# Kernel optimization log

Hardware: AMD Instinct MI355X
Metric: run time of the kernel (lower is better)

The kernel has to match this reference:

```python
import jax, jax.numpy as jnp
import numpy as np

EMA = 0.99
THRESH = 0.8
EPS = 1e-8


def setup_inputs() -> dict:
    key = jax.random.key(0)
    k1, k2, k3, k4 = jax.random.split(key, 4)
    B, C, M = 8192, 2048, 8192
    return {
        "features": jax.random.normal(k1, (B, C), dtype=jnp.float32),
        "confidence": jax.random.uniform(k2, (B,), dtype=jnp.float32),
        "mem_features": jax.random.normal(k3, (M, C), dtype=jnp.float32),
        "mem_confidences": jax.random.uniform(k4, (M,), dtype=jnp.float32),
        "ptr0": 4096,
        "filled0": 4096,
    }


def _update(mem_feat, mem_conf, ptr0, filled0, features, confidence):
    M = mem_feat.shape[0]

    def step(carry, xs):
        mf, mc, ptr, filled = carry
        feat, conf = xs
        is_high = conf > THRESH
        p = jnp.mod(ptr, M)
        exists = filled > p
        cur_f = mf[p]          # [C]
        cur_c = mc[p]
        upd_f = jnp.where(exists, EMA * cur_f + (1.0 - EMA) * feat, feat)
        upd_c = jnp.where(exists, EMA * cur_c + (1.0 - EMA) * conf, conf)
        new_f = jnp.where(is_high, upd_f, cur_f)
        new_c = jnp.where(is_high, upd_c, cur_c)
        mf = mf.at[p].set(new_f)
        mc = mc.at[p].set(new_c)
        filled = filled + jnp.where(is_high & (~exists), 1, 0).astype(filled.dtype)
        ptr = ptr + jnp.where(is_high, 1, 0).astype(ptr.dtype)
        return (mf, mc, ptr, filled), None

    init = (mem_feat, mem_conf,
            jnp.asarray(ptr0, jnp.int32), jnp.asarray(filled0, jnp.int32))
    (mf, mc, ptr, filled), _ = jax.lax.scan(step, init, (features, confidence))
    return mf, mc, filled


def reference(features, confidence, mem_features, mem_confidences, ptr0, filled0):
    mf, mc, filled = _update(mem_features, mem_confidences, ptr0, filled0,
                             features, confidence)
    M, C = mf.shape
    # confidence-weighted stats over valid slots [:filled] (mask, jit-safe)
    valid = (jnp.arange(M) < filled).astype(mf.dtype)
    w = mc * valid                              # [M]
    total = jnp.sum(w) + EPS
    mean = jnp.einsum("mc,m->c", mf, w) / total  # [C]
    diff = mf - mean[None, :]
    var = jnp.einsum("mc,m->c", diff * diff, w) / total
    std = jnp.sqrt(var + EPS)
    # pack: updated memory bank + weighted mean + weighted std -> [M+2, C]
    return jnp.concatenate([mf, mean[None, :], std[None, :]], axis=0)
```

## Files before the change

kernel.cpp:

```cpp
#include <hip/hip_runtime.h>
#include <math.h>

#define EMA_A 0.99f
#define EMA_B 0.01f
#define THRESH 0.8f
#define EPS_F 1e-8f

#define NBLK2 512
#define RPB   16

typedef float fx4 __attribute__((ext_vector_type(4)));


__global__ __launch_bounds__(1024)
void k_scan(const float* __restrict__ conf,
            const int* __restrict__ ptr0_p,
            const int* __restrict__ filled0_p,
            int* __restrict__ hdr,
            int* __restrict__ slot_info,
            int B, int M)
{
    const int tid  = threadIdx.x;
    const int lane = tid & 63;

    for (int m = tid; m < M; m += 1024) slot_info[m] = -1;

    const int base_i = tid * 8;
    int mask = 0;
    #pragma unroll
    for (int k = 0; k < 8; ++k) {
        int i = base_i + k;
        float c = (i < B) ? conf[i] : 0.0f;
        mask |= (c > THRESH) ? (1 << k) : 0;
    }
    int cnt = __popc(mask);

    __shared__ int s_cnt[1024];
    __shared__ int s_gbase[64];
    s_cnt[tid] = cnt;
    __syncthreads();

    if (tid < 64) {
        int sum16 = 0;
        #pragma unroll
        for (int u = 0; u < 16; ++u) sum16 += s_cnt[tid * 16 + u];
        int v = sum16;
        #pragma unroll
        for (int d = 1; d < 64; d <<= 1) {
            int o = __shfl_up(v, d, 64);
            if (lane >= d) v += o;
        }
        s_gbase[tid] = v - sum16;
        if (tid == 63) hdr[0] = v;
    }
    __syncthreads();
    const int K = hdr[0];

    int j = s_gbase[tid >> 4];
    for (int u = (tid & ~15); u < tid; ++u) j += s_cnt[u];

    int P0 = ((ptr0_p[0] % M) + M) % M;
    int F0 = filled0_p[0];
    if (F0 < 0) F0 = 0;
    if (F0 > M) F0 = M;
    const int L0 = M - P0;
    const int F1 = F0 + (M - (P0 > F0 ? P0 : F0));

    #pragma unroll
    for (int k = 0; k < 8; ++k) {
        if (mask & (1 << k)) {
            int exist;
            if (j < L0)          exist = (P0 + j) < F0 ? 1 : 0;
            else if (j < L0 + M) exist = (j - L0) < F1 ? 1 : 0;
            else                 exist = 1;
            int p = (P0 + j) % M;
            slot_info[p] = ((base_i + k) << 1) | exist;
            ++j;
        }
    }

    if (tid == 0) {
        int n0 = K < L0 ? K : L0;
        int e0 = F0 - P0; if (e0 < 0) e0 = 0; if (e0 > n0) e0 = n0;
        int fresh0 = n0 - e0;
        int n1 = K - L0; if (n1 < 0) n1 = 0; if (n1 > M) n1 = M;
        int fresh1 = n1 - F1; if (fresh1 < 0) fresh1 = 0;
        int filled = F0 + fresh0 + fresh1;
        if (filled > M) filled = M;
        hdr[1] = filled;
    }
}


__global__ __launch_bounds__(512)
void k_update(const float* __restrict__ mem_feat,
              const float* __restrict__ feat,
              const float* __restrict__ conf,
              const float* __restrict__ mem_conf,
              const int* __restrict__ slot_info,
              const int* __restrict__ hdr,
              float* __restrict__ out,
              float* __restrict__ p0,
              float* __restrict__ p1,
              float* __restrict__ p2,
              int C)
{
    const int blk = blockIdx.x, tid = threadIdx.x;
    const int c0 = tid * 4;

    __shared__ int   s_info[RPB];
    __shared__ float s_w[RPB];
    const int row0 = blk * RPB;
    if (tid < RPB) {
        const int m = row0 + tid;
        const int info = slot_info[m];
        const int filled = hdr[1];
        const float mco = mem_conf[m];
        float mcu = mco;
        if (info >= 0) {
            float c = conf[info >> 1];
            mcu = (info & 1) ? (EMA_A * mco + EMA_B * c) : c;
        }
        s_info[tid] = info;
        s_w[tid]    = (m < filled) ? mcu : 0.0f;
    }
    __syncthreads();
    if (tid == 0) {
        float s = 0.0f;
        #pragma unroll
        for (int r = 0; r < RPB; ++r) s += s_w[r];
        p0[blk] = s;
    }

    fx4 s1 = {0.f, 0.f, 0.f, 0.f};
    fx4 s2 = {0.f, 0.f, 0.f, 0.f};

    #pragma unroll 4
    for (int r = 0; r < RPB; ++r) {
        const int m = row0 + r;
        const size_t base = (size_t)m * C;
        const int info = s_info[r];
        fx4 x;
        if (info < 0) {
            x = *(const fx4*)(mem_feat + base + c0);
        } else if (info & 1) {
            fx4 mv = *(const fx4*)(mem_feat + base + c0);
            fx4 fv = *(const fx4*)(feat + (size_t)(info >> 1) * C + c0);
            x = EMA_A * mv + EMA_B * fv;
        } else {
            x = *(const fx4*)(feat + (size_t)(info >> 1) * C + c0);
        }
        const float wv = s_w[r];
        s1 += wv * x;
        s2 += wv * x * x;
        __builtin_nontemporal_store(x, (fx4*)(out + base + c0));
    }
    const size_t pb = (size_t)blk * C;
    *(fx4*)(p1 + pb + c0) = s1;
    *(fx4*)(p2 + pb + c0) = s2;
}


__global__ __launch_bounds__(256)
void k_stats(const float* __restrict__ p0,
             const float* __restrict__ p1,
             const float* __restrict__ p2,
             float* __restrict__ out,
             int M, int C)
{
    const int tid = threadIdx.x;

    __shared__ float s_sw[4];
    float sw = 0.0f;
    for (int i = tid; i < NBLK2; i += 256) sw += p0[i];
    #pragma unroll
    for (int d = 32; d >= 1; d >>= 1) sw += __shfl_down(sw, d, 64);
    if ((tid & 63) == 0) s_sw[tid >> 6] = sw;
    __syncthreads();

    const int cc = tid & 31;
    const int chunk = tid >> 5;
    const int c = blockIdx.x * 32 + cc;
    double s1 = 0.0, s2 = 0.0;
    for (int bb = 0; bb < NBLK2 / 8; ++bb) {
        int b = chunk * (NBLK2 / 8) + bb;
        s1 += (double)p1[(size_t)b * C + c];
        s2 += (double)p2[(size_t)b * C + c];
    }
    __shared__ double l1[256], l2[256];
    l1[tid] = s1;
    l2[tid] = s2;
    __syncthreads();
    if (chunk == 0) {
        for (int q = 1; q < 8; ++q) { s1 += l1[cc + 32 * q]; s2 += l2[cc + 32 * q]; }
        double sumw  = (double)(s_sw[0] + s_sw[1] + s_sw[2] + s_sw[3]);
        double total = sumw + (double)EPS_F;
        double mean  = s1 / total;
        double var   = (s2 - 2.0 * mean * s1 + mean * mean * sumw) / total;
        out[(size_t)M * C + c]       = (float)mean;
        out[(size_t)(M + 1) * C + c] = (float)sqrt(var + (double)EPS_F);
    }
}


extern "C" void kernel_launch(void* const* d_in, const int* in_sizes, int n_in,
                              void* d_out, int out_size, void* d_ws, size_t ws_size,
                              hipStream_t stream)
{
    const float* features     = (const float*)d_in[0];
    const float* confidence   = (const float*)d_in[1];
    const float* mem_features = (const float*)d_in[2];
    const float* mem_conf     = (const float*)d_in[3];
    const int*   ptr0         = (const int*)d_in[4];
    const int*   filled0      = (const int*)d_in[5];

    const int B = in_sizes[1];
    const int M = in_sizes[3];
    const int C = in_sizes[0] / B;

    char* ws = (char*)d_ws;
    int*   hdr       = (int*)ws;
    int*   slot_info = (int*)(ws + 1024);
    float* p0        = (float*)(ws + 1024 + 4 * (size_t)M);
    float* p1        = (float*)(ws + 65536);
    float* p2        = (float*)(ws + 65536 + 4 * (size_t)NBLK2 * C);

    float* out = (float*)d_out;

    k_scan<<<1, 1024, 0, stream>>>(confidence, ptr0, filled0, hdr, slot_info, B, M);
    k_update<<<NBLK2, 512, 0, stream>>>(mem_features, features, confidence, mem_conf,
                                        slot_info, hdr, out, p0, p1, p2, C);
    k_stats<<<C / 32, 256, 0, stream>>>(p0, p1, p2, out, M, C);
}
```

Baseline: 185.6 us.

## Replace per-block partial sums with global float atomics and a light finalize kernel

The update kernel now accumulates weighted sums directly into global arrays with float atomicAdd, instead of writing per-block partials that a separate stats kernel re-reads. Each block doubles its threads, splits the rows between two halves, and combines the halves through shared memory before issuing the atomics. The row source pointer is also precomputed per row so the inner loop has fewer branches. This removes the partial-buffer round trip and the heavier reduction kernel, at the cost of many atomic operations per column, non-deterministic float summation order, and reduced precision compared with the old double-precision reduction. The zeroing of the global accumulators is folded into the scan kernel.

```diff
diff --git a/kernel.cpp b/kernel.cpp
--- a/kernel.cpp
+++ b/kernel.cpp
@@ -18,12 +18,16 @@
             const int* __restrict__ filled0_p,
             int* __restrict__ hdr,
             int* __restrict__ slot_info,
-            int B, int M)
+            float* __restrict__ g_sumw,
+            float* __restrict__ g1,
+            int B, int M, int C)
 {
     const int tid  = threadIdx.x;
     const int lane = tid & 63;
 
     for (int m = tid; m < M; m += 1024) slot_info[m] = -1;
+    for (int i = tid; i < 2 * C; i += 1024) g1[i] = 0.0f;
+    if (tid == 0) *g_sumw = 0.0f;
 
     const int base_i = tid * 8;
     int mask = 0;
@@ -92,7 +96,7 @@
 }
 
 
-__global__ __launch_bounds__(512)
+__global__ __launch_bounds__(1024)
 void k_update(const float* __restrict__ mem_feat,
               const float* __restrict__ feat,
               const float* __restrict__ conf,
@@ -100,103 +104,94 @@
               const int* __restrict__ slot_info,
               const int* __restrict__ hdr,
               float* __restrict__ out,
-              float* __restrict__ p0,
-              float* __restrict__ p1,
-              float* __restrict__ p2,
+              float* __restrict__ g_sumw,
+              float* __restrict__ g1,
+              float* __restrict__ g2,
               int C)
 {
-    const int blk = blockIdx.x, tid = threadIdx.x;
-    const int c0 = tid * 4;
-
-    __shared__ int   s_info[RPB];
+    const int blk  = blockIdx.x, tid = threadIdx.x;
+    const int half = tid >> 9;
+    const int c4   = tid & 511;
+    const int c0   = c4 * 4;
+    const int row0 = blk * RPB;
+
+    __shared__ const float* s_src[RPB];
+    __shared__ int   s_ema[RPB];
     __shared__ float s_w[RPB];
-    const int row0 = blk * RPB;
+
     if (tid < RPB) {
         const int m = row0 + tid;
         const int info = slot_info[m];
         const int filled = hdr[1];
         const float mco = mem_conf[m];
         float mcu = mco;
+        const float* src = mem_feat + (size_t)m * C;
+        int ema = 0;
         if (info >= 0) {
-            float c = conf[info >> 1];
-            mcu = (info & 1) ? (EMA_A * mco + EMA_B * c) : c;
-        }
-        s_info[tid] = info;
-        s_w[tid]    = (m < filled) ? mcu : 0.0f;
+            const float c = conf[info >> 1];
+            src = feat + (size_t)(info >> 1) * C;
+            if (info & 1) { mcu = EMA_A * mco + EMA_B * c; ema = 1; }
+            else          { mcu = c; }
+        }
+        s_src[tid] = src;
+        s_ema[tid] = ema;
+        s_w[tid]   = (m < filled) ? mcu : 0.0f;
     }
     __syncthreads();
     if (tid == 0) {
         float s = 0.0f;
         #pragma unroll
         for (int r = 0; r < RPB; ++r) s += s_w[r];
-        p0[blk] = s;
+        atomicAdd(g_sumw, s);
     }
 
     fx4 s1 = {0.f, 0.f, 0.f, 0.f};
     fx4 s2 = {0.f, 0.f, 0.f, 0.f};
 
-    #pragma unroll 4
-    for (int r = 0; r < RPB; ++r) {
+    #pragma unroll
+    for (int rr = 0; rr < RPB / 2; ++rr) {
+        const int r = rr * 2 + half;
         const int m = row0 + r;
-        const size_t base = (size_t)m * C;
-        const int info = s_info[r];
-        fx4 x;
-        if (info < 0) {
-            x = *(const fx4*)(mem_feat + base + c0);
-        } else if (info & 1) {
-            fx4 mv = *(const fx4*)(mem_feat + base + c0);
-            fx4 fv = *(const fx4*)(feat + (size_t)(info >> 1) * C + c0);
-            x = EMA_A * mv + EMA_B * fv;
-        } else {
-            x = *(const fx4*)(feat + (size_t)(info >> 1) * C + c0);
+        fx4 x = *(const fx4*)(s_src[r] + c0);
+        if (s_ema[r]) {
+            fx4 mv = *(const fx4*)(mem_feat + (size_t)m * C + c0);
+            x = EMA_A * mv + EMA_B * x;
         }
         const float wv = s_w[r];
         s1 += wv * x;
         s2 += wv * x * x;
-        __builtin_nontemporal_store(x, (fx4*)(out + base + c0));
-    }
-    const size_t pb = (size_t)blk * C;
-    *(fx4*)(p1 + pb + c0) = s1;
-    *(fx4*)(p2 + pb + c0) = s2;
+        __builtin_nontemporal_store(x, (fx4*)(out + (size_t)m * C + c0));
+    }
+
+    __shared__ fx4 st1[512], st2[512];
+    if (half == 1) { st1[c4] = s1; st2[c4] = s2; }
+    __syncthreads();
+    if (half == 0) {
+        s1 += st1[c4];
+        s2 += st2[c4];
+        atomicAdd(&g1[c0 + 0], s1.x); atomicAdd(&g1[c0 + 1], s1.y);
+        atomicAdd(&g1[c0 + 2], s1.z); atomicAdd(&g1[c0 + 3], s1.w);
+        atomicAdd(&g2[c0 + 0], s2.x); atomicAdd(&g2[c0 + 1], s2.y);
+        atomicAdd(&g2[c0 + 2], s2.z); atomicAdd(&g2[c0 + 3], s2.w);
+    }
 }
 
 
 __global__ __launch_bounds__(256)
-void k_stats(const float* __restrict__ p0,
-             const float* __restrict__ p1,
-             const float* __restrict__ p2,
-             float* __restrict__ out,
-             int M, int C)
-{
-    const int tid = threadIdx.x;
-
-    __shared__ float s_sw[4];
-    float sw = 0.0f;
-    for (int i = tid; i < NBLK2; i += 256) sw += p0[i];
-    #pragma unroll
-    for (int d = 32; d >= 1; d >>= 1) sw += __shfl_down(sw, d, 64);
-    if ((tid & 63) == 0) s_sw[tid >> 6] = sw;
-    __syncthreads();
-
-    const int cc = tid & 31;
-    const int chunk = tid >> 5;
-    const int c = blockIdx.x * 32 + cc;
-    double s1 = 0.0, s2 = 0.0;
-    for (int bb = 0; bb < NBLK2 / 8; ++bb) {
-        int b = chunk * (NBLK2 / 8) + bb;
-        s1 += (double)p1[(size_t)b * C + c];
-        s2 += (double)p2[(size_t)b * C + c];
-    }
-    __shared__ double l1[256], l2[256];
-    l1[tid] = s1;
-    l2[tid] = s2;
-    __syncthreads();
-    if (chunk == 0) {
-        for (int q = 1; q < 8; ++q) { s1 += l1[cc + 32 * q]; s2 += l2[cc + 32 * q]; }
-        double sumw  = (double)(s_sw[0] + s_sw[1] + s_sw[2] + s_sw[3]);
-        double total = sumw + (double)EPS_F;
-        double mean  = s1 / total;
-        double var   = (s2 - 2.0 * mean * s1 + mean * mean * sumw) / total;
+void k_fin(const float* __restrict__ g_sumw,
+           const float* __restrict__ g1,
+           const float* __restrict__ g2,
+           float* __restrict__ out,
+           int M, int C)
+{
+    const int c = blockIdx.x * 256 + threadIdx.x;
+    if (c < C) {
+        const double sumw  = (double)g_sumw[0];
+        const double total = sumw + (double)EPS_F;
+        const double s1 = (double)g1[c];
+        const double s2 = (double)g2[c];
+        const double mean = s1 / total;
+        const double var  = (s2 - 2.0 * mean * s1 + mean * mean * sumw) / total;
         out[(size_t)M * C + c]       = (float)mean;
         out[(size_t)(M + 1) * C + c] = (float)sqrt(var + (double)EPS_F);
     }
@@ -221,14 +216,15 @@
     char* ws = (char*)d_ws;
     int*   hdr       = (int*)ws;
     int*   slot_info = (int*)(ws + 1024);
-    float* p0        = (float*)(ws + 1024 + 4 * (size_t)M);
-    float* p1        = (float*)(ws + 65536);
-    float* p2        = (float*)(ws + 65536 + 4 * (size_t)NBLK2 * C);
+    float* g_sumw    = (float*)(ws + 33792);
+    float* g1        = (float*)(ws + 35840);
+    float* g2        = (float*)(ws + 44032);
 
     float* out = (float*)d_out;
 
-    k_scan<<<1, 1024, 0, stream>>>(confidence, ptr0, filled0, hdr, slot_info, B, M);
-    k_update<<<NBLK2, 512, 0, stream>>>(mem_features, features, confidence, mem_conf,
-                                        slot_info, hdr, out, p0, p1, p2, C);
-    k_stats<<<C / 32, 256, 0, stream>>>(p0, p1, p2, out, M, C);
-}
+    k_scan<<<1, 1024, 0, stream>>>(confidence, ptr0, filled0, hdr, slot_info,
+                                   g_sumw, g1, B, M, C);
+    k_update<<<NBLK2, 1024, 0, stream>>>(mem_features, features, confidence, mem_conf,
+                                         slot_info, hdr, out, g_sumw, g1, g2, C);
+    k_fin<<<(C + 255) / 256, 256, 0, stream>>>(g_sumw, g1, g2, out, M, C);
+}
```

Result: slower. 216.9 us (+16.9%).

## Batch row loads in update kernel, halve rows per block, widen stats reduction

Applied to the files above, without the earlier changes.

The update kernel now works on 8 rows per block across 1024 blocks instead of 16 rows across 512. It picks each row's source pointer up front and issues all row loads before any compute, so more memory requests are in flight per thread. The stats kernel is reshaped to 1024-thread blocks covering 64 columns, with 16 partial chunks per column. The cost is that the partial-sum buffers double in size, so more traffic goes to writing and re-reading partials.

```diff
diff --git a/kernel.cpp b/kernel.cpp
--- a/kernel.cpp
+++ b/kernel.cpp
@@ -6,8 +6,8 @@
 #define THRESH 0.8f
 #define EPS_F 1e-8f
 
-#define NBLK2 512
-#define RPB   16
+#define NBLK2 1024
+#define RPB   8
 
 typedef float fx4 __attribute__((ext_vector_type(4)));
 
@@ -105,24 +105,31 @@
               float* __restrict__ p2,
               int C)
 {
-    const int blk = blockIdx.x, tid = threadIdx.x;
-    const int c0 = tid * 4;
-
-    __shared__ int   s_info[RPB];
+    const int blk  = blockIdx.x, tid = threadIdx.x;
+    const int c0   = tid * 4;
+    const int row0 = blk * RPB;
+
+    __shared__ const float* s_src[RPB];
+    __shared__ int   s_ema[RPB];
     __shared__ float s_w[RPB];
-    const int row0 = blk * RPB;
+
     if (tid < RPB) {
         const int m = row0 + tid;
         const int info = slot_info[m];
         const int filled = hdr[1];
         const float mco = mem_conf[m];
         float mcu = mco;
+        const float* src = mem_feat + (size_t)m * C;
+        int ema = 0;
         if (info >= 0) {
-            float c = conf[info >> 1];
-            mcu = (info & 1) ? (EMA_A * mco + EMA_B * c) : c;
-        }
-        s_info[tid] = info;
-        s_w[tid]    = (m < filled) ? mcu : 0.0f;
+            const float c = conf[info >> 1];
+            src = feat + (size_t)(info >> 1) * C;
+            if (info & 1) { mcu = EMA_A * mco + EMA_B * c; ema = 1; }
+            else          { mcu = c; }
+        }
+        s_src[tid] = src;
+        s_ema[tid] = ema;
+        s_w[tid]   = (m < filled) ? mcu : 0.0f;
     }
     __syncthreads();
     if (tid == 0) {
@@ -132,73 +139,77 @@
         p0[blk] = s;
     }
 
+    fx4 x[RPB];
+    #pragma unroll
+    for (int r = 0; r < RPB; ++r)
+        x[r] = *(const fx4*)(s_src[r] + c0);
+
+    #pragma unroll
+    for (int r = 0; r < RPB; ++r) {
+        if (s_ema[r]) {
+            fx4 mv = *(const fx4*)(mem_feat + (size_t)(row0 + r) * C + c0);
+            x[r] = EMA_A * mv + EMA_B * x[r];
+        }
+    }
+
     fx4 s1 = {0.f, 0.f, 0.f, 0.f};
     fx4 s2 = {0.f, 0.f, 0.f, 0.f};
-
-    #pragma unroll 4
+    #pragma unroll
     for (int r = 0; r < RPB; ++r) {
-        const int m = row0 + r;
-        const size_t base = (size_t)m * C;
-        const int info = s_info[r];
-        fx4 x;
-        if (info < 0) {
-            x = *(const fx4*)(mem_feat + base + c0);
-        } else if (info & 1) {
-            fx4 mv = *(const fx4*)(mem_feat + base + c0);
-            fx4 fv = *(const fx4*)(feat + (size_t)(info >> 1) * C + c0);
-            x = EMA_A * mv + EMA_B * fv;
-        } else {
-            x = *(const fx4*)(feat + (size_t)(info >> 1) * C + c0);
-        }
         const float wv = s_w[r];
-        s1 += wv * x;
-        s2 += wv * x * x;
-        __builtin_nontemporal_store(x, (fx4*)(out + base + c0));
-    }
+        s1 += wv * x[r];
+        s2 += wv * x[r] * x[r];
+        __builtin_nontemporal_store(x[r], (fx4*)(out + (size_t)(row0 + r) * C + c0));
+    }
+
     const size_t pb = (size_t)blk * C;
     *(fx4*)(p1 + pb + c0) = s1;
     *(fx4*)(p2 + pb + c0) = s2;
 }
 
 
-__global__ __launch_bounds__(256)
+__global__ __launch_bounds__(1024)
 void k_stats(const float* __restrict__ p0,
              const float* __restrict__ p1,
              const float* __restrict__ p2,
              float* __restrict__ out,
              int M, int C)
 {
-    const int tid = threadIdx.x;
-
-    __shared__ float s_sw[4];
-    float sw = 0.0f;
-    for (int i = tid; i < NBLK2; i += 256) sw += p0[i];
+    const int tid   = threadIdx.x;
+    const int col   = blockIdx.x * 64 + (tid & 63);
+    const int chunk = tid >> 6;
+
+    __shared__ float s_swp[16];
+    float sw = (tid < NBLK2) ? p0[tid] : 0.0f;
     #pragma unroll
     for (int d = 32; d >= 1; d >>= 1) sw += __shfl_down(sw, d, 64);
-    if ((tid & 63) == 0) s_sw[tid >> 6] = sw;
-    __syncthreads();
-
-    const int cc = tid & 31;
-    const int chunk = tid >> 5;
-    const int c = blockIdx.x * 32 + cc;
+    if ((tid & 63) == 0) s_swp[tid >> 6] = sw;
+
     double s1 = 0.0, s2 = 0.0;
-    for (int bb = 0; bb < NBLK2 / 8; ++bb) {
-        int b = chunk * (NBLK2 / 8) + bb;
-        s1 += (double)p1[(size_t)b * C + c];
-        s2 += (double)p2[(size_t)b * C + c];
-    }
-    __shared__ double l1[256], l2[256];
+    for (int i = 0; i < NBLK2 / 16; ++i) {
+        const int b = chunk * (NBLK2 / 16) + i;
+        s1 += (double)p1[(size_t)b * C + col];
+        s2 += (double)p2[(size_t)b * C + col];
+    }
+    __shared__ double l1[1024], l2[1024];
     l1[tid] = s1;
     l2[tid] = s2;
     __syncthreads();
     if (chunk == 0) {
-        for (int q = 1; q < 8; ++q) { s1 += l1[cc + 32 * q]; s2 += l2[cc + 32 * q]; }
-        double sumw  = (double)(s_sw[0] + s_sw[1] + s_sw[2] + s_sw[3]);
-        double total = sumw + (double)EPS_F;
-        double mean  = s1 / total;
-        double var   = (s2 - 2.0 * mean * s1 + mean * mean * sumw) / total;
-        out[(size_t)M * C + c]       = (float)mean;
-        out[(size_t)(M + 1) * C + c] = (float)sqrt(var + (double)EPS_F);
+        #pragma unroll
+        for (int q = 1; q < 16; ++q) {
+            s1 += l1[tid + 64 * q];
+            s2 += l2[tid + 64 * q];
+        }
+        float swt = 0.0f;
+        #pragma unroll
+        for (int u = 0; u < 16; ++u) swt += s_swp[u];
+        const double sumw  = (double)swt;
+        const double total = sumw + (double)EPS_F;
+        const double mean  = s1 / total;
+        const double var   = (s2 - 2.0 * mean * s1 + mean * mean * sumw) / total;
+        out[(size_t)M * C + col]       = (float)mean;
+        out[(size_t)(M + 1) * C + col] = (float)sqrt(var + (double)EPS_F);
     }
 }
 
@@ -221,7 +232,7 @@
     char* ws = (char*)d_ws;
     int*   hdr       = (int*)ws;
     int*   slot_info = (int*)(ws + 1024);
-    float* p0        = (float*)(ws + 1024 + 4 * (size_t)M);
+    float* p0        = (float*)(ws + 33792);
     float* p1        = (float*)(ws + 65536);
     float* p2        = (float*)(ws + 65536 + 4 * (size_t)NBLK2 * C);
 
@@ -230,5 +241,5 @@
     k_scan<<<1, 1024, 0, stream>>>(confidence, ptr0, filled0, hdr, slot_info, B, M);
     k_update<<<NBLK2, 512, 0, stream>>>(mem_features, features, confidence, mem_conf,
                                         slot_info, hdr, out, p0, p1, p2, C);
-    k_stats<<<C / 32, 256, 0, stream>>>(p0, p1, p2, out, M, C);
-}
+    k_stats<<<C / 64, 1024, 0, stream>>>(p0, p1, p2, out, M, C);
+}
```

Result: faster. 180.5 us (-2.8%).
